# Kernel tuning notes

Measured on AMD Instinct MI355X. Metric: run time of the kernel, lower is better.

Reference implementation:

```python
import jax, jax.numpy as jnp
import numpy as np

B, N, E = 4, 10000, 160000
F_IN, D_ATT, H = 64, 128, 8
D_K = D_ATT // H  # 16


def setup_inputs() -> dict:
    key = jax.random.key(0)
    ks = jax.random.split(key, 8)
    x = jax.random.normal(ks[0], (B, N, F_IN), dtype=jnp.float32)
    edge = jax.random.randint(ks[1], (2, E), 0, N, dtype=jnp.int64)
    scale = 0.05
    Qw = jax.random.normal(ks[2], (D_ATT, F_IN), dtype=jnp.float32) * scale
    Qb = jnp.zeros((D_ATT,), dtype=jnp.float32)
    Kw = jax.random.normal(ks[3], (D_ATT, F_IN), dtype=jnp.float32) * scale
    Kb = jnp.zeros((D_ATT,), dtype=jnp.float32)
    Vw = jax.random.normal(ks[4], (D_ATT, F_IN), dtype=jnp.float32) * scale
    Vb = jnp.zeros((D_ATT,), dtype=jnp.float32)
    return {"x": x, "Qw": Qw, "Qb": Qb, "Kw": Kw, "Kb": Kb, "Vw": Vw, "Vb": Vb, "edge": edge}


def _proj(x, W, b):
    # x: (B, N, F_IN) -> (B, N, D_K, H)  (view to (B,N,H,D_K) then transpose(2,3))
    y = jnp.einsum('bnf,af->bna', x, W) + b  # (B, N, D_ATT)
    y = y.reshape(y.shape[0], y.shape[1], H, D_K)
    return jnp.swapaxes(y, 2, 3)  # (B, N, D_K, H)


def reference(x, Qw, Qb, Kw, Kb, Vw, Vb, edge):
    q = _proj(x, Qw, Qb)  # (B, N, D_K, H)
    k = _proj(x, Kw, Kb)
    v = _proj(x, Vw, Vb)
    src = q[:, edge[0], :, :]    # (B, E, D_K, H) gather by source node
    dst_k = k[:, edge[1], :, :]  # (B, E, D_K, H) gather by dest node
    prods = jnp.sum(src * dst_k, axis=2) / np.float32(np.sqrt(D_K))  # (B, E, H)
    attention = jax.nn.softmax(prods, axis=1)  # softmax over the edge dimension, as in original
    return attention, v
```

## Files before the change

kernel.cpp:

```cpp
#include <hip/hip_runtime.h>
#include <hip/hip_bf16.h>

constexpr int B  = 4;
constexpr int N  = 10000;
constexpr int E  = 160000;
constexpr int F  = 64;
constexpr int DA = 128;
constexpr int H  = 8;
constexpr int DK = 16;
constexpr int TOTAL = B * N;

constexpr int EPB  = 256;
constexpr int NBLK = E / EPB;

typedef __attribute__((ext_vector_type(8))) short short8v;
typedef __attribute__((ext_vector_type(4))) float f32x4;
typedef __attribute__((ext_vector_type(2))) float f32x2;

__device__ __forceinline__ unsigned pack_bf16(float a, float b) {
    unsigned ua = __builtin_bit_cast(unsigned, a);
    unsigned ub = __builtin_bit_cast(unsigned, b);
    ua = (ua + 0x7fffu + ((ua >> 16) & 1u)) >> 16;
    ub = (ub + 0x7fffu + ((ub >> 16) & 1u)) >> 16;
    return ua | (ub << 16);
}
__device__ __forceinline__ short8v cvt8(float4 a, float4 b) {
    union { unsigned u[4]; short8v s; } r;
    r.u[0] = pack_bf16(a.x, a.y);
    r.u[1] = pack_bf16(a.z, a.w);
    r.u[2] = pack_bf16(b.x, b.y);
    r.u[3] = pack_bf16(b.z, b.w);
    return r.s;
}
__device__ __forceinline__ void fp8dot(unsigned q, unsigned k, f32x2& olo, f32x2& ohi) {
    f32x2 ql = __builtin_amdgcn_cvt_pk_f32_fp8((int)q, false);
    f32x2 qh = __builtin_amdgcn_cvt_pk_f32_fp8((int)q, true);
    f32x2 kl = __builtin_amdgcn_cvt_pk_f32_fp8((int)k, false);
    f32x2 kh = __builtin_amdgcn_cvt_pk_f32_fp8((int)k, true);
    olo += ql * kl;
    ohi += qh * kh;
}

__global__ __launch_bounds__(256) void proj_mfma(
    const float* __restrict__ x,
    const float* __restrict__ Qw, const float* __restrict__ Kw,
    const float* __restrict__ Vw,
    const float* __restrict__ Qb, const float* __restrict__ Kb,
    const float* __restrict__ Vb,
    unsigned char* __restrict__ qws, unsigned char* __restrict__ kws,
    float* __restrict__ vout)
{
    __shared__ unsigned char wlds[3 * DA * F * 2];

    const int t = threadIdx.x;

    #pragma unroll
    for (int j = 0; j < 12; ++j) {
        const float* W = (j < 4) ? Qw : (j < 8) ? Kw : Vw;
        const float sc = (j < 4) ? 0.25f : 1.0f;
        const int A = j * 4096 + t * 16;
        const int foff = (A - (j / 4) * 16384) / 4;
        const float4* s4 = (const float4*)(W + foff * 2);
        float4 v0 = s4[0], v1 = s4[1];
        uint4 v;
        v.x = pack_bf16(v0.x * sc, v0.y * sc);
        v.y = pack_bf16(v0.z * sc, v0.w * sc);
        v.z = pack_bf16(v1.x * sc, v1.y * sc);
        v.w = pack_bf16(v1.z * sc, v1.w * sc);
        *(uint4*)(wlds + (A ^ (((A >> 7) & 7) << 4))) = v;
    }
    __syncthreads();

    const int w = t >> 6, lane = t & 63;
    const int tn = lane & 15, g = lane >> 4;

    const int m0t = blockIdx.x * 64 + w * 16;

    const float4* xr = (const float4*)(x + (size_t)(m0t + tn) * F);
    const short8v a0 = cvt8(xr[g * 2],     xr[g * 2 + 1]);
    const short8v a1 = cvt8(xr[8 + g * 2], xr[8 + g * 2 + 1]);

    const int sw = (tn & 7) << 4;

    #pragma unroll
    for (int mat = 0; mat < 3; ++mat) {
        const float* bias = (mat == 0) ? Qb : (mat == 1) ? Kb : Vb;
        const float bsc = (mat == 0) ? 0.25f : 1.0f;
        const unsigned char* wm = wlds + mat * (DA * F * 2);

        f32x4 acc[8];
        #pragma unroll
        for (int a0t = 0; a0t < 8; ++a0t) {
            const float bb = bias[a0t * 16 + tn] * bsc;
            acc[a0t][0] = bb; acc[a0t][1] = bb;
            acc[a0t][2] = bb; acc[a0t][3] = bb;
        }
        #pragma unroll
        for (int a0t = 0; a0t < 8; ++a0t) {
            const int rowb = (a0t * 16 + tn) * 128;
            short8v b0 = *(const short8v*)(wm + ((rowb + g * 16) ^ sw));
            short8v b1 = *(const short8v*)(wm + ((rowb + 64 + g * 16) ^ sw));
            acc[a0t] = __builtin_amdgcn_mfma_f32_16x16x32_bf16(a0, b0, acc[a0t], 0, 0, 0);
            acc[a0t] = __builtin_amdgcn_mfma_f32_16x16x32_bf16(a1, b1, acc[a0t], 0, 0, 0);
        }

        if (mat < 2) {
            unsigned char* qk_dst = (mat == 0) ? qws : kws;
            #pragma unroll
            for (int r = 0; r < 4; ++r) {
                const int node = m0t + g * 4 + r;
                unsigned u0 = (unsigned)__builtin_amdgcn_cvt_pk_fp8_f32(
                                  acc[0][r], acc[1][r], 0, false);
                u0 = (unsigned)__builtin_amdgcn_cvt_pk_fp8_f32(
                                  acc[2][r], acc[3][r], (int)u0, true);
                unsigned u1 = (unsigned)__builtin_amdgcn_cvt_pk_fp8_f32(
                                  acc[4][r], acc[5][r], 0, false);
                u1 = (unsigned)__builtin_amdgcn_cvt_pk_fp8_f32(
                                  acc[6][r], acc[7][r], (int)u1, true);
                *(uint2*)(qk_dst + (size_t)node * DA + tn * 8) = make_uint2(u0, u1);
            }
        } else {
            #pragma unroll
            for (int r = 0; r < 4; ++r) {
                const int node = m0t + g * 4 + r;
                float* vb = vout + (size_t)node * DA + tn * 8;
                *(float4*)vb       = make_float4(acc[0][r], acc[1][r], acc[2][r], acc[3][r]);
                *(float4*)(vb + 4) = make_float4(acc[4][r], acc[5][r], acc[6][r], acc[7][r]);
            }
        }
    }
}

__global__ __launch_bounds__(256) void gather_dot_sm(
    const unsigned char* __restrict__ qws, const unsigned char* __restrict__ kws,
    const int* __restrict__ edge, float* __restrict__ att,
    float* __restrict__ psum)
{
    const int b   = blockIdx.x;
    const int blk = blockIdx.y;
    const int t = threadIdx.x;
    const int w = t >> 6, lane = t & 63;
    const int g = lane >> 2, i = lane & 3;

    const unsigned char* qb = qws + (size_t)b * N * DA;
    const unsigned char* kb = kws + (size_t)b * N * DA;
    float* attb = att + (size_t)b * E * H;

    const int ew0 = blk * EPB + w * 64;

    const int i0 = ew0 + lane;
    const int s0p = edge[i0];
    const int d0p = edge[E + i0];

    float sa0 = 0.f, sa1 = 0.f;

    #pragma unroll
    for (int r = 0; r < 4; ++r) {
        const int el = ew0 + r * 16 + g;
        const int srcl = r * 16 + g;
        const int s = __shfl(s0p, srcl);
        const int d = __shfl(d0p, srcl);
        const uint4* qp = (const uint4*)(qb + (size_t)s * DA) + i;
        const uint4* kp = (const uint4*)(kb + (size_t)d * DA) + i;
        uint4 q0 = qp[0], q1 = qp[4];
        uint4 k0 = kp[0], k1 = kp[4];

        f32x2 o01 = {0.f, 0.f}, o23 = {0.f, 0.f}, o45 = {0.f, 0.f}, o67 = {0.f, 0.f};
        fp8dot(q0.x, k0.x, o01, o23);
        fp8dot(q0.y, k0.y, o45, o67);
        fp8dot(q0.z, k0.z, o01, o23);
        fp8dot(q0.w, k0.w, o45, o67);
        fp8dot(q1.x, k1.x, o01, o23);
        fp8dot(q1.y, k1.y, o45, o67);
        fp8dot(q1.z, k1.z, o01, o23);
        fp8dot(q1.w, k1.w, o45, o67);

        #pragma unroll
        for (int off = 1; off <= 2; off <<= 1) {
            o01[0] += __shfl_xor(o01[0], off);  o01[1] += __shfl_xor(o01[1], off);
            o23[0] += __shfl_xor(o23[0], off);  o23[1] += __shfl_xor(o23[1], off);
            o45[0] += __shfl_xor(o45[0], off);  o45[1] += __shfl_xor(o45[1], off);
            o67[0] += __shfl_xor(o67[0], off);  o67[1] += __shfl_xor(o67[1], off);
        }

        f32x2 pp = (i == 0) ? o01 : (i == 1) ? o23 : (i == 2) ? o45 : o67;
        float e0 = __expf(pp[0]), e1 = __expf(pp[1]);
        *(f32x2*)(attb + (size_t)el * H + 2 * i) = f32x2{e0, e1};
        sa0 += e0;
        sa1 += e1;
    }

    #pragma unroll
    for (int off = 4; off <= 32; off <<= 1) {
        sa0 += __shfl_xor(sa0, off);
        sa1 += __shfl_xor(sa1, off);
    }

    __shared__ float2 red[4][4];
    if (g == 0) red[w][i] = make_float2(sa0, sa1);
    __syncthreads();
    if (t < 4) {
        float s0f = 0.f, s1f = 0.f;
        #pragma unroll
        for (int ww = 0; ww < 4; ++ww) {
            float2 v = red[ww][t];
            s0f += v.x;
            s1f += v.y;
        }
        psum[((size_t)b * H + 2 * t)     * NBLK + blk] = s0f;
        psum[((size_t)b * H + 2 * t + 1) * NBLK + blk] = s1f;
    }
}

__global__ __launch_bounds__(256) void softmax_norm(
    float* __restrict__ att, const float* __restrict__ psum)
{
    const int b   = blockIdx.x;
    const int blk = blockIdx.y;
    const int t = threadIdx.x;
    const int w = t >> 6, lane = t & 63;

    __shared__ float inv[H];
    {
        const float* p0 = psum + ((size_t)b * H + 2 * w) * NBLK;
        const float* p1 = psum + ((size_t)b * H + 2 * w + 1) * NBLK;
        float s0 = 0.f, s1 = 0.f;
        for (int c = lane; c < NBLK; c += 64) {
            s0 += p0[c];
            s1 += p1[c];
        }
        #pragma unroll
        for (int off = 1; off < 64; off <<= 1) {
            s0 += __shfl_xor(s0, off);
            s1 += __shfl_xor(s1, off);
        }
        if (lane == 0) {
            inv[2 * w]     = 1.0f / s0;
            inv[2 * w + 1] = 1.0f / s1;
        }
    }
    __syncthreads();

    float* p = att + (size_t)b * (E * H) + (size_t)blk * (EPB * H) + t * 8;
    float4 v0 = *(float4*)p;
    float4 v1 = *(float4*)(p + 4);
    v0.x *= inv[0]; v0.y *= inv[1]; v0.z *= inv[2]; v0.w *= inv[3];
    v1.x *= inv[4]; v1.y *= inv[5]; v1.z *= inv[6]; v1.w *= inv[7];
    *(float4*)p       = v0;
    *(float4*)(p + 4) = v1;
}

extern "C" void kernel_launch(void* const* d_in, const int* in_sizes, int n_in,
                              void* d_out, int out_size, void* d_ws, size_t ws_size,
                              hipStream_t stream)
{
    const float* x  = (const float*)d_in[0];
    const float* Qw = (const float*)d_in[1];
    const float* Qb = (const float*)d_in[2];
    const float* Kw = (const float*)d_in[3];
    const float* Kb = (const float*)d_in[4];
    const float* Vw = (const float*)d_in[5];
    const float* Vb = (const float*)d_in[6];
    const int*   edge = (const int*)d_in[7];

    float* out  = (float*)d_out;
    float* att  = out;
    float* vout = out + (size_t)B * E * H;

    char* w = (char*)d_ws;
    unsigned char* qws = (unsigned char*)w;
    unsigned char* kws = qws + (size_t)B * N * DA;
    float* psum = (float*)(w + 2 * (size_t)B * N * DA);

    hipLaunchKernelGGL(proj_mfma, dim3(TOTAL / 64), dim3(256), 0, stream,
                       x, Qw, Kw, Vw, Qb, Kb, Vb, qws, kws, vout);
    hipLaunchKernelGGL(gather_dot_sm, dim3(B, NBLK), dim3(256), 0, stream,
                       qws, kws, edge, att, psum);
    hipLaunchKernelGGL(softmax_norm, dim3(B, NBLK), dim3(256), 0, stream,
                       att, psum);
}
```

Baseline: 46.90 us.

## Precompute softmax denominators in separate kernel and hoist x loads before weight staging

The per-block reduction of partial sums, which every one of the 2500 normalize blocks previously repeated redundantly, is moved into a tiny kernel that computes the B*H inverse denominators once. The normalize kernel then just reads eight scalars and scales its slice, with no barrier. Separately, the projection kernel issues its x loads before the LDS weight staging so the global latency overlaps with the weight conversion. The cost is one extra kernel launch and a dependency on a tiny serial kernel.

```diff
diff --git a/kernel.cpp b/kernel.cpp
--- a/kernel.cpp
+++ b/kernel.cpp
@@ -53,6 +53,13 @@
     __shared__ unsigned char wlds[3 * DA * F * 2];
 
     const int t = threadIdx.x;
+    const int w = t >> 6, lane = t & 63;
+    const int tn = lane & 15, g = lane >> 4;
+    const int m0t = blockIdx.x * 64 + w * 16;
+
+    const float4* xr = (const float4*)(x + (size_t)(m0t + tn) * F);
+    const float4 x0 = xr[g * 2], x1 = xr[g * 2 + 1];
+    const float4 x2 = xr[8 + g * 2], x3 = xr[8 + g * 2 + 1];
 
     #pragma unroll
     for (int j = 0; j < 12; ++j) {
@@ -71,14 +78,8 @@
     }
     __syncthreads();
 
-    const int w = t >> 6, lane = t & 63;
-    const int tn = lane & 15, g = lane >> 4;
-
-    const int m0t = blockIdx.x * 64 + w * 16;
-
-    const float4* xr = (const float4*)(x + (size_t)(m0t + tn) * F);
-    const short8v a0 = cvt8(xr[g * 2],     xr[g * 2 + 1]);
-    const short8v a1 = cvt8(xr[8 + g * 2], xr[8 + g * 2 + 1]);
+    const short8v a0 = cvt8(x0, x1);
+    const short8v a1 = cvt8(x2, x3);
 
     const int sw = (tn & 7) << 4;
 
@@ -212,40 +213,34 @@
     }
 }
 
+__global__ __launch_bounds__(64) void softmax_final(
+    const float* __restrict__ psum, float* __restrict__ MS)
+{
+    const int bh = blockIdx.x;
+    const int t = threadIdx.x;
+    float s = 0.f;
+    for (int c = t; c < NBLK; c += 64) s += psum[(size_t)bh * NBLK + c];
+    #pragma unroll
+    for (int off = 1; off < 64; off <<= 1) s += __shfl_xor(s, off);
+    if (t == 0) MS[bh] = 1.0f / s;
+}
+
 __global__ __launch_bounds__(256) void softmax_norm(
-    float* __restrict__ att, const float* __restrict__ psum)
+    float* __restrict__ att, const float* __restrict__ MS)
 {
     const int b   = blockIdx.x;
     const int blk = blockIdx.y;
     const int t = threadIdx.x;
-    const int w = t >> 6, lane = t & 63;
-
-    __shared__ float inv[H];
-    {
-        const float* p0 = psum + ((size_t)b * H + 2 * w) * NBLK;
-        const float* p1 = psum + ((size_t)b * H + 2 * w + 1) * NBLK;
-        float s0 = 0.f, s1 = 0.f;
-        for (int c = lane; c < NBLK; c += 64) {
-            s0 += p0[c];
-            s1 += p1[c];
-        }
-        #pragma unroll
-        for (int off = 1; off < 64; off <<= 1) {
-            s0 += __shfl_xor(s0, off);
-            s1 += __shfl_xor(s1, off);
-        }
-        if (lane == 0) {
-            inv[2 * w]     = 1.0f / s0;
-            inv[2 * w + 1] = 1.0f / s1;
-        }
-    }
-    __syncthreads();
+
+    const float* ms = MS + b * H;
+    const float i0 = ms[0], i1 = ms[1], i2 = ms[2], i3 = ms[3];
+    const float i4 = ms[4], i5 = ms[5], i6 = ms[6], i7 = ms[7];
 
     float* p = att + (size_t)b * (E * H) + (size_t)blk * (EPB * H) + t * 8;
     float4 v0 = *(float4*)p;
     float4 v1 = *(float4*)(p + 4);
-    v0.x *= inv[0]; v0.y *= inv[1]; v0.z *= inv[2]; v0.w *= inv[3];
-    v1.x *= inv[4]; v1.y *= inv[5]; v1.z *= inv[6]; v1.w *= inv[7];
+    v0.x *= i0; v0.y *= i1; v0.z *= i2; v0.w *= i3;
+    v1.x *= i4; v1.y *= i5; v1.z *= i6; v1.w *= i7;
     *(float4*)p       = v0;
     *(float4*)(p + 4) = v1;
 }
@@ -271,11 +266,14 @@
     unsigned char* qws = (unsigned char*)w;
     unsigned char* kws = qws + (size_t)B * N * DA;
     float* psum = (float*)(w + 2 * (size_t)B * N * DA);
+    float* MS   = psum + (size_t)B * H * NBLK;
 
     hipLaunchKernelGGL(proj_mfma, dim3(TOTAL / 64), dim3(256), 0, stream,
                        x, Qw, Kw, Vw, Qb, Kb, Vb, qws, kws, vout);
     hipLaunchKernelGGL(gather_dot_sm, dim3(B, NBLK), dim3(256), 0, stream,
                        qws, kws, edge, att, psum);
+    hipLaunchKernelGGL(softmax_final, dim3(B * H), dim3(64), 0, stream,
+                       psum, MS);
     hipLaunchKernelGGL(softmax_norm, dim3(B, NBLK), dim3(256), 0, stream,
-                       att, psum);
-}
+                       att, MS);
+}
```

New measurement: 47.29 us. No clear change (+0.8%).

## Store unnormalized exponentials as bf16 in workspace and hoist x loads before weight staging

Applied to the files above, without the earlier changes.

The gather kernel now writes the unnormalized exp scores to a separate workspace packed as bf16 instead of fp32 in the output. The normalization kernel reads them back, unpacks them, scales by the inverse sums and writes fp32 output. This halves the intermediate write and read traffic, at the cost of bf16 rounding on the attention values. The projection kernel also issues its x loads before staging weights into LDS, and computes the V matrix first so its global stores can overlap with the rest.

```diff
diff --git a/kernel.cpp b/kernel.cpp
--- a/kernel.cpp
+++ b/kernel.cpp
@@ -24,6 +24,14 @@
     ub = (ub + 0x7fffu + ((ub >> 16) & 1u)) >> 16;
     return ua | (ub << 16);
 }
+__device__ __forceinline__ float bf16lo(unsigned u) {
+    u <<= 16;
+    return __builtin_bit_cast(float, u);
+}
+__device__ __forceinline__ float bf16hi(unsigned u) {
+    u &= 0xffff0000u;
+    return __builtin_bit_cast(float, u);
+}
 __device__ __forceinline__ short8v cvt8(float4 a, float4 b) {
     union { unsigned u[4]; short8v s; } r;
     r.u[0] = pack_bf16(a.x, a.y);
@@ -53,6 +61,13 @@
     __shared__ unsigned char wlds[3 * DA * F * 2];
 
     const int t = threadIdx.x;
+    const int w = t >> 6, lane = t & 63;
+    const int tn = lane & 15, g = lane >> 4;
+    const int m0t = blockIdx.x * 64 + w * 16;
+
+    const float4* xr = (const float4*)(x + (size_t)(m0t + tn) * F);
+    const float4 x0 = xr[g * 2], x1 = xr[g * 2 + 1];
+    const float4 x2 = xr[8 + g * 2], x3 = xr[8 + g * 2 + 1];
 
     #pragma unroll
     for (int j = 0; j < 12; ++j) {
@@ -71,19 +86,14 @@
     }
     __syncthreads();
 
-    const int w = t >> 6, lane = t & 63;
-    const int tn = lane & 15, g = lane >> 4;
-
-    const int m0t = blockIdx.x * 64 + w * 16;
-
-    const float4* xr = (const float4*)(x + (size_t)(m0t + tn) * F);
-    const short8v a0 = cvt8(xr[g * 2],     xr[g * 2 + 1]);
-    const short8v a1 = cvt8(xr[8 + g * 2], xr[8 + g * 2 + 1]);
+    const short8v a0 = cvt8(x0, x1);
+    const short8v a1 = cvt8(x2, x3);
 
     const int sw = (tn & 7) << 4;
 
     #pragma unroll
-    for (int mat = 0; mat < 3; ++mat) {
+    for (int it = 0; it < 3; ++it) {
+        const int mat = (it == 0) ? 2 : (it == 1) ? 0 : 1;
         const float* bias = (mat == 0) ? Qb : (mat == 1) ? Kb : Vb;
         const float bsc = (mat == 0) ? 0.25f : 1.0f;
         const unsigned char* wm = wlds + mat * (DA * F * 2);
@@ -133,7 +143,7 @@
 
 __global__ __launch_bounds__(256) void gather_dot_sm(
     const unsigned char* __restrict__ qws, const unsigned char* __restrict__ kws,
-    const int* __restrict__ edge, float* __restrict__ att,
+    const int* __restrict__ edge, unsigned* __restrict__ expws,
     float* __restrict__ psum)
 {
     const int b   = blockIdx.x;
@@ -144,7 +154,7 @@
 
     const unsigned char* qb = qws + (size_t)b * N * DA;
     const unsigned char* kb = kws + (size_t)b * N * DA;
-    float* attb = att + (size_t)b * E * H;
+    unsigned* expb = expws + (size_t)b * E * (H / 2);
 
     const int ew0 = blk * EPB + w * 64;
 
@@ -185,7 +195,7 @@
 
         f32x2 pp = (i == 0) ? o01 : (i == 1) ? o23 : (i == 2) ? o45 : o67;
         float e0 = __expf(pp[0]), e1 = __expf(pp[1]);
-        *(f32x2*)(attb + (size_t)el * H + 2 * i) = f32x2{e0, e1};
+        expb[(size_t)el * 4 + i] = pack_bf16(e0, e1);
         sa0 += e0;
         sa1 += e1;
     }
@@ -213,7 +223,8 @@
 }
 
 __global__ __launch_bounds__(256) void softmax_norm(
-    float* __restrict__ att, const float* __restrict__ psum)
+    const unsigned* __restrict__ expws, float* __restrict__ att,
+    const float* __restrict__ psum)
 {
     const int b   = blockIdx.x;
     const int blk = blockIdx.y;
@@ -241,11 +252,14 @@
     }
     __syncthreads();
 
-    float* p = att + (size_t)b * (E * H) + (size_t)blk * (EPB * H) + t * 8;
-    float4 v0 = *(float4*)p;
-    float4 v1 = *(float4*)(p + 4);
-    v0.x *= inv[0]; v0.y *= inv[1]; v0.z *= inv[2]; v0.w *= inv[3];
-    v1.x *= inv[4]; v1.y *= inv[5]; v1.z *= inv[6]; v1.w *= inv[7];
+    const int el = blk * EPB + t;
+    const uint4 u = ((const uint4*)(expws + (size_t)b * E * 4))[el];
+    float* p = att + ((size_t)b * E + el) * H;
+    float4 v0, v1;
+    v0.x = bf16lo(u.x) * inv[0];  v0.y = bf16hi(u.x) * inv[1];
+    v0.z = bf16lo(u.y) * inv[2];  v0.w = bf16hi(u.y) * inv[3];
+    v1.x = bf16lo(u.z) * inv[4];  v1.y = bf16hi(u.z) * inv[5];
+    v1.z = bf16lo(u.w) * inv[6];  v1.w = bf16hi(u.w) * inv[7];
     *(float4*)p       = v0;
     *(float4*)(p + 4) = v1;
 }
@@ -270,12 +284,13 @@
     char* w = (char*)d_ws;
     unsigned char* qws = (unsigned char*)w;
     unsigned char* kws = qws + (size_t)B * N * DA;
-    float* psum = (float*)(w + 2 * (size_t)B * N * DA);
+    unsigned* expws = (unsigned*)(w + 2 * (size_t)B * N * DA);
+    float* psum = (float*)(expws + (size_t)B * E * 4);
 
     hipLaunchKernelGGL(proj_mfma, dim3(TOTAL / 64), dim3(256), 0, stream,
                        x, Qw, Kw, Vw, Qb, Kb, Vb, qws, kws, vout);
     hipLaunchKernelGGL(gather_dot_sm, dim3(B, NBLK), dim3(256), 0, stream,
-                       qws, kws, edge, att, psum);
+                       qws, kws, edge, expws, psum);
     hipLaunchKernelGGL(softmax_norm, dim3(B, NBLK), dim3(256), 0, stream,
-                       att, psum);
-}
+                       expws, att, psum);
+}
```

After: 43.81 us. 1.07x faster.
